# Performance work log

Measured on AMD Instinct MI355X. Metric: run time of the kernel, lower is better.

Reference implementation:

```python
import jax, jax.numpy as jnp
import numpy as np

B, C, F, J = 64, 16, 2048, 25
EMBED, CLASSES, NJ = 64, 5, 12
AFFECT = slice(0, 12)
UNAFFECT = slice(12, 24)


def setup_inputs() -> dict:
    key = jax.random.key(0)
    k0, k1, k2, k3 = jax.random.split(key, 4)
    features = jax.random.normal(k0, (B, C, F, J), dtype=jnp.float32)
    W1 = jax.random.normal(k1, (EMBED, C, NJ), dtype=jnp.float32) * 0.05
    b1 = jnp.zeros((EMBED,), jnp.float32)
    W2 = jax.random.normal(k2, (EMBED, C, NJ), dtype=jnp.float32) * 0.05
    b2 = jnp.zeros((EMBED,), jnp.float32)
    Wl = jax.random.normal(k3, (CLASSES, 16 * EMBED), dtype=jnp.float32) * 0.02
    bl = jnp.zeros((CLASSES,), jnp.float32)
    return {"features": features, "W1": W1, "b1": b1, "W2": W2, "b2": b2, "Wl": Wl, "bl": bl}


def _stat_features(x, proto):
    # x: [b, c, f, j]; single sort shared by min/max/quantiles/median
    f = x.shape[-2]
    xs = jnp.sort(x, axis=-2)

    def quant(p):
        # torch.quantile linear interpolation
        pos = p * (f - 1)
        lo = int(np.floor(pos)); hi = int(np.ceil(pos)); frac = np.float32(pos - lo)
        return xs[..., lo, :] * (1.0 - frac) + xs[..., hi, :] * frac

    s1 = xs[..., 0, :]                       # min
    s2 = xs[..., -1, :]                      # max
    s3 = quant(0.25)
    s4 = xs[..., (f - 1) // 2, :]            # torch.median: lower middle element
    s5 = quant(0.75)
    s6 = jnp.mean(x, axis=-2)
    s7 = jnp.std(x, axis=-2, ddof=1)         # torch.std unbiased
    s8 = s2 - s1
    z = (x - s6[..., None, :]) / s7[..., None, :]
    if proto:
        s9 = jnp.mean(z ** 3, axis=-2)       # skew
    else:
        s9 = jnp.mean(z ** 4, axis=-2) - 3.0  # excess kurtosis
    return jnp.stack([s2, s3, s4, s5, s6, s7, s8, s9], axis=-2)  # [b, c, 8, j]


def _fuse(stat, W, b):
    # Conv2d kernel (1, joints) == contraction over (c, j) per stat row
    out = jnp.einsum('bcsj,ecj->bes', stat, W) + b[None, :, None]
    return out.reshape(out.shape[0], -1)  # flatten (embed, stats) like torch.flatten


def reference(features, W1, b1, W2, b2, Wl, bl):
    affected = features[:, :, :, AFFECT]
    unaffected = features[:, :, :, UNAFFECT]
    stat_af = _stat_features(affected, proto=False)
    stat_ua = _stat_features(unaffected, proto=False)
    # attn=False path (STAT_VA block disabled)
    stat1 = _stat_features(unaffected + affected, proto=True)
    _ = _fuse(stat1, W1, b1)  # stat1 branch only feeds CL loss (get_cl_loss=False)
    stat2 = jnp.concatenate([stat_af, stat_ua], axis=-2)  # [b, c, 16, j]
    flat2 = _fuse(stat2, W2, b2)                          # [b, 16*embed]
    logits = flat2 @ Wl.T + bl
    return logits
```

## Files before the change

### kernel.cpp

```cpp
#include <hip/hip_runtime.h>
#include <hip/hip_bf16.h>
#include <math.h>


#define F_LEN 2048
#define JTOT 25
#define STATS_PER_BC 192
#define LP 2056

__device__ __forceinline__ int swz(int i) {
  return (i & ~31) | ((i + ((i >> 5) << 2)) & 31);
}

template <int PAT>
__device__ __forceinline__ float ds_swz(float v) {
  return __int_as_float(
      __builtin_amdgcn_ds_swizzle(__float_as_int(v), PAT));
}
__device__ __forceinline__ float swzxor(float v, const int lm) {
  switch (lm) {
    case 1:  return ds_swz<0x041F>(v);
    case 2:  return ds_swz<0x081F>(v);
    case 4:  return ds_swz<0x101F>(v);
    case 8:  return ds_swz<0x201F>(v);
    default: return ds_swz<0x401F>(v);
  }
}
__device__ __forceinline__ float wave_sum(float v, int addr32) {
  v += ds_swz<0x041F>(v);
  v += ds_swz<0x081F>(v);
  v += ds_swz<0x101F>(v);
  v += ds_swz<0x201F>(v);
  v += ds_swz<0x401F>(v);
  v += __int_as_float(
      __builtin_amdgcn_ds_bpermute(addr32, __float_as_int(v)));
  return v;
}

__global__ __launch_bounds__(256) void stat_kernel(
    const float* __restrict__ Fp, float* __restrict__ stat2) {
  __shared__ float lds[4 * LP];
  const int g = blockIdx.x;
  const int xcd = g & 7;
  const int mm = g >> 3;
  const int bc = xcd * 128 + mm / 6;
  const int grp = mm % 6;
  const int t = threadIdx.x;
  const int w = t >> 6;
  const int lane = t & 63;
  const int addr32 = ((lane ^ 32) << 2);
  const int j0 = grp * 4;
  float* wlds = lds + w * LP;

  {
    const float* bbase = Fp + (size_t)bc * F_LEN * JTOT + j0;
    const int f0 = t >> 2, jj = t & 3;
    float* ldst = lds + jj * LP;
#pragma unroll
    for (int it = 0; it < 32; ++it) {
      const int f = it * 64 + f0;
      ldst[swz(f)] = bbase[(size_t)f * JTOT + jj];
    }
  }
  __syncthreads();

  float x[32];
  {
    const float4* src4 = (const float4*)wlds;
#pragma unroll
    for (int q = 0; q < 8; ++q) {
      float4 v = src4[lane * 8 + ((lane + q) & 7)];
      x[4 * q] = v.x; x[4 * q + 1] = v.y;
      x[4 * q + 2] = v.z; x[4 * q + 3] = v.w;
    }
  }

  float sum = 0.f;
#pragma unroll
  for (int e = 0; e < 32; ++e) sum += x[e];
  sum = wave_sum(sum, addr32);
  const float m = sum * (1.0f / 2048.0f);

  float c2 = 0.f, c4 = 0.f;
#pragma unroll
  for (int e = 0; e < 32; ++e) {
    float d = x[e] - m;
    float dd = d * d;
    c2 += dd;
    c4 += dd * dd;
  }
  c2 = wave_sum(c2, addr32);
  c4 = wave_sum(c4, addr32);
  const float var = c2 * (1.0f / 2047.0f);
  const float sd = sqrtf(var);
  const float kurt = (c4 * (1.0f / 2048.0f)) / (var * var) - 3.0f;

#pragma unroll
  for (int kp = 1; kp <= 4; ++kp) {
    const int k = 1 << kp;
#pragma unroll
    for (int jp = kp - 1; jp >= 0; --jp) {
      const int st = 1 << jp;
#pragma unroll
      for (int e = 0; e < 32; ++e) {
        if ((e & st) == 0) {
          const bool up = ((e & k) == 0);
          float a = x[e], b = x[e + st];
          float lo2 = fminf(a, b), hi2 = fmaxf(a, b);
          x[e] = up ? lo2 : hi2;
          x[e + st] = up ? hi2 : lo2;
        }
      }
    }
  }

  unsigned Fst = 0u;
#pragma unroll
  for (int kp = 5; kp <= 10; ++kp) {
    const unsigned d = ((lane >> (kp - 5)) & 1) ? 0x80000000u : 0u;
#pragma unroll
    for (int jp = kp - 1; jp >= 5; --jp) {
      const int lm = 1 << (jp - 5);
      const unsigned r = ((lane >> (jp - 5)) & 1) ? 0x80000000u : 0u;
      const unsigned tgt = d ^ r;
      const unsigned fl = tgt ^ Fst;
      Fst = tgt;
#pragma unroll
      for (int e = 0; e < 32; ++e)
        x[e] = __uint_as_float(__float_as_uint(x[e]) ^ fl);
#pragma unroll
      for (int e = 0; e < 32; ++e) {
        float o = swzxor(x[e], lm);
        x[e] = fminf(x[e], -o);
      }
    }
    {
      const unsigned fl = d ^ Fst;
      Fst = d;
#pragma unroll
      for (int e = 0; e < 32; ++e)
        x[e] = __uint_as_float(__float_as_uint(x[e]) ^ fl);
    }
#pragma unroll
    for (int jp = (kp - 1 < 4 ? kp - 1 : 4); jp >= 0; --jp) {
      const int st = 1 << jp;
#pragma unroll
      for (int e = 0; e < 32; ++e) {
        if ((e & st) == 0) {
          float a = x[e], b = x[e + st];
          x[e] = fminf(a, b);
          x[e + st] = fmaxf(a, b);
        }
      }
    }
  }
#pragma unroll
  for (int e = 0; e < 32; ++e)
    x[e] = __uint_as_float(__float_as_uint(x[e]) ^ Fst);

  {
    float4* dst4 = (float4*)wlds;
#pragma unroll
    for (int q = 0; q < 8; ++q) {
      int wq = 8 * lane + ((q + lane) & 7);
      dst4[wq] = make_float4(x[4 * q], x[4 * q + 1], x[4 * q + 2], x[4 * q + 3]);
    }
  }

  const int kk = (lane == 0) ? 511
               : (lane == 1) ? 512
               : (lane == 2) ? 1023
               : (lane == 3) ? 1535 : 1536;
  const int mtot = kk + 1;
  int lo = mtot - 1024; if (lo < 0) lo = 0;
  int hi = (mtot < 1024) ? mtot : 1024;
  for (int it = 0; it < 11; ++it) {
    const bool act = lo < hi;
    const int s = (lo + hi) >> 1;
    const int sa = (s < 1023) ? s : 1023;
    float Av = wlds[swz(sa)];
    Av = (s < 1024) ? Av : INFINITY;
    int bidx = mtot - s - 1;
    bidx = bidx < 0 ? 0 : (bidx > 1023 ? 1023 : bidx);
    const float Bv = wlds[swz(2047 - bidx)];
    const bool gg = act && (Bv > Av);
    if (gg) lo = s + 1;
    else if (act) hi = s;
  }
  float val;
  {
    const int s = lo;
    const int ia = (s - 1 < 0) ? 0 : s - 1;
    const float fa = wlds[swz(ia)];
    const float fromA = (s > 0) ? fa : -INFINITY;
    const int bi = mtot - s - 1;
    const int ib = (bi < 0) ? 0 : bi;
    const float fb = wlds[swz(2047 - ib)];
    const float fromB = (bi >= 0) ? fb : -INFINITY;
    val = fmaxf(fromA, fromB);
  }

  const float a511  = __shfl(val, 0, 64);
  const float a512  = __shfl(val, 1, 64);
  const float amed  = __shfl(val, 2, 64);
  const float a1535 = __shfl(val, 3, 64);
  const float a1536 = __shfl(val, 4, 64);

  if (lane == 0) {
    const float mn = fminf(wlds[swz(0)], wlds[swz(2047)]);
    const float mx = fmaxf(wlds[swz(1023)], wlds[swz(1024)]);
    const float q25 = 0.25f * a511 + 0.75f * a512;
    const float q75 = 0.75f * a1535 + 0.25f * a1536;
    const int j = j0 + w;
    const int jj = (j < 12) ? j : j - 12;
    const int sb = (j < 12) ? 0 : 8;
    float st8[8] = {mx, q25, amed, q75, m, sd, mx - mn, kurt};
    float* o = stat2 + (bc * 16 + sb) * 12 + jj;
#pragma unroll
    for (int s2 = 0; s2 < 8; ++s2) o[s2 * 12] = st8[s2];
  }
}

__global__ __launch_bounds__(256) void fuse_kernel(
    const float* __restrict__ stat2, const float* __restrict__ W2,
    const float* __restrict__ b2, const float* __restrict__ Wl,
    const float* __restrict__ bl, float* __restrict__ out) {
  __shared__ float s_stat[16 * STATS_PER_BC];
  __shared__ float s_flat[1024];
  __shared__ float s_red[4];

  const int b = blockIdx.x;
  const int t = threadIdx.x;

  for (int idx = t; idx < 16 * STATS_PER_BC; idx += 256)
    s_stat[idx] = stat2[b * (16 * STATS_PER_BC) + idx];
  __syncthreads();

  const int e = t & 63;
  const int q = t >> 6;
  float acc[4] = {0.f, 0.f, 0.f, 0.f};
  for (int c = 0; c < 16; ++c) {
    const float* wrow = W2 + (e * 16 + c) * 12;
    const float* srow = s_stat + c * STATS_PER_BC;
#pragma unroll
    for (int jj = 0; jj < 12; ++jj) {
      const float wv = wrow[jj];
#pragma unroll
      for (int ss = 0; ss < 4; ++ss)
        acc[ss] += srow[(q * 4 + ss) * 12 + jj] * wv;
    }
  }
  const float bb = b2[e];
#pragma unroll
  for (int ss = 0; ss < 4; ++ss)
    s_flat[e * 16 + q * 4 + ss] = acc[ss] + bb;
  __syncthreads();

  for (int k = 0; k < 5; ++k) {
    float p = 0.f;
    for (int i = t; i < 1024; i += 256) p += s_flat[i] * Wl[k * 1024 + i];
#pragma unroll
    for (int off = 32; off; off >>= 1) p += __shfl_down(p, off, 64);
    if ((t & 63) == 0) s_red[t >> 6] = p;
    __syncthreads();
    if (t == 0)
      out[b * 5 + k] = s_red[0] + s_red[1] + s_red[2] + s_red[3] + bl[k];
    __syncthreads();
  }
}

extern "C" void kernel_launch(void* const* d_in, const int* in_sizes, int n_in,
                              void* d_out, int out_size, void* d_ws,
                              size_t ws_size, hipStream_t stream) {
  const float* Fp = (const float*)d_in[0];
  const float* W2 = (const float*)d_in[3];
  const float* b2 = (const float*)d_in[4];
  const float* Wl = (const float*)d_in[5];
  const float* bl = (const float*)d_in[6];
  float* out = (float*)d_out;

  float* stat2 = (float*)d_ws;

  stat_kernel<<<6144, 256, 0, stream>>>(Fp, stat2);
  fuse_kernel<<<64, 256, 0, stream>>>(stat2, W2, b2, Wl, bl, out);
}
```

Before: 440.3 us.

## Complete full bitonic sort in registers and drop LDS merge-path quantile search

The bitonic network now runs one more stage across the whole wave, using ds_bpermute for the lane-xor-32 exchange, so all 2048 values end up fully sorted in registers. Order statistics are then read with direct shuffles instead of writing the data back to LDS and doing a merge-path binary search. The load phase now uses vector float4 global reads into a half-sized LDS buffer filled in two passes, and launch bounds request 8 blocks per CU. The aim is to cut LDS footprint and serial search latency and raise occupancy, at the price of an extra full sort stage using a slower cross-half permute.

Result: slower. 462.7 us (+5.1%).

```diff
diff --git a/kernel.cpp b/kernel.cpp
--- a/kernel.cpp
+++ b/kernel.cpp
@@ -8,6 +8,8 @@
 #define STATS_PER_BC 192
 #define LP 2056
 
+typedef float f4a __attribute__((ext_vector_type(4), aligned(4)));
+
 __device__ __forceinline__ int swz(int i) {
   return (i & ~31) | ((i + ((i >> 5) << 2)) & 31);
 }
@@ -17,13 +19,16 @@
   return __int_as_float(
       __builtin_amdgcn_ds_swizzle(__float_as_int(v), PAT));
 }
-__device__ __forceinline__ float swzxor(float v, const int lm) {
+__device__ __forceinline__ float swzxor(float v, const int lm,
+                                        const int addr32) {
   switch (lm) {
     case 1:  return ds_swz<0x041F>(v);
     case 2:  return ds_swz<0x081F>(v);
     case 4:  return ds_swz<0x101F>(v);
     case 8:  return ds_swz<0x201F>(v);
-    default: return ds_swz<0x401F>(v);
+    case 16: return ds_swz<0x401F>(v);
+    default: return __int_as_float(
+        __builtin_amdgcn_ds_bpermute(addr32, __float_as_int(v)));
   }
 }
 __device__ __forceinline__ float wave_sum(float v, int addr32) {
@@ -37,9 +42,22 @@
   return v;
 }
 
-__global__ __launch_bounds__(256) void stat_kernel(
+__device__ __forceinline__ void read_x(const float* wlds, int lane,
+                                       float* x) {
+  const float4* src4 = (const float4*)wlds;
+#pragma unroll
+  for (int q = 0; q < 8; ++q) {
+    float4 v = src4[lane * 8 + ((lane + q) & 7)];
+    x[4 * q] = v.x;
+    x[4 * q + 1] = v.y;
+    x[4 * q + 2] = v.z;
+    x[4 * q + 3] = v.w;
+  }
+}
+
+__global__ __launch_bounds__(256, 8) void stat_kernel(
     const float* __restrict__ Fp, float* __restrict__ stat2) {
-  __shared__ float lds[4 * LP];
+  __shared__ float lds[2 * LP];
   const int g = blockIdx.x;
   const int xcd = g & 7;
   const int mm = g >> 3;
@@ -50,30 +68,37 @@
   const int lane = t & 63;
   const int addr32 = ((lane ^ 32) << 2);
   const int j0 = grp * 4;
-  float* wlds = lds + w * LP;
-
+
+  float vz[8], vw[8];
+  const int rot = (t + ((t >> 5) << 2)) & 31;
+  float* p0 = lds + (t & ~31) + rot;
   {
     const float* bbase = Fp + (size_t)bc * F_LEN * JTOT + j0;
-    const int f0 = t >> 2, jj = t & 3;
-    float* ldst = lds + jj * LP;
-#pragma unroll
-    for (int it = 0; it < 32; ++it) {
-      const int f = it * 64 + f0;
-      ldst[swz(f)] = bbase[(size_t)f * JTOT + jj];
+#pragma unroll
+    for (int it = 0; it < 8; ++it) {
+      const int f = it * 256 + t;
+      f4a v = *reinterpret_cast<const f4a*>(bbase + (size_t)f * JTOT);
+      p0[it * 256] = v.x;
+      p0[LP + it * 256] = v.y;
+      vz[it] = v.z;
+      vw[it] = v.w;
     }
   }
   __syncthreads();
 
   float x[32];
+  if (w < 2) read_x(lds + w * LP, lane, x);
+  __syncthreads();
+
   {
-    const float4* src4 = (const float4*)wlds;
-#pragma unroll
-    for (int q = 0; q < 8; ++q) {
-      float4 v = src4[lane * 8 + ((lane + q) & 7)];
-      x[4 * q] = v.x; x[4 * q + 1] = v.y;
-      x[4 * q + 2] = v.z; x[4 * q + 3] = v.w;
-    }
-  }
+#pragma unroll
+    for (int it = 0; it < 8; ++it) {
+      p0[it * 256] = vz[it];
+      p0[LP + it * 256] = vw[it];
+    }
+  }
+  __syncthreads();
+  if (w >= 2) read_x(lds + (w - 2) * LP, lane, x);
 
   float sum = 0.f;
 #pragma unroll
@@ -116,7 +141,7 @@
 
   unsigned Fst = 0u;
 #pragma unroll
-  for (int kp = 5; kp <= 10; ++kp) {
+  for (int kp = 5; kp <= 11; ++kp) {
     const unsigned d = ((lane >> (kp - 5)) & 1) ? 0x80000000u : 0u;
 #pragma unroll
     for (int jp = kp - 1; jp >= 5; --jp) {
@@ -130,7 +155,7 @@
         x[e] = __uint_as_float(__float_as_uint(x[e]) ^ fl);
 #pragma unroll
       for (int e = 0; e < 32; ++e) {
-        float o = swzxor(x[e], lm);
+        float o = swzxor(x[e], lm, addr32);
         x[e] = fminf(x[e], -o);
       }
     }
@@ -142,7 +167,7 @@
         x[e] = __uint_as_float(__float_as_uint(x[e]) ^ fl);
     }
 #pragma unroll
-    for (int jp = (kp - 1 < 4 ? kp - 1 : 4); jp >= 0; --jp) {
+    for (int jp = 4; jp >= 0; --jp) {
       const int st = 1 << jp;
 #pragma unroll
       for (int e = 0; e < 32; ++e) {
@@ -154,61 +179,16 @@
       }
     }
   }
-#pragma unroll
-  for (int e = 0; e < 32; ++e)
-    x[e] = __uint_as_float(__float_as_uint(x[e]) ^ Fst);
-
-  {
-    float4* dst4 = (float4*)wlds;
-#pragma unroll
-    for (int q = 0; q < 8; ++q) {
-      int wq = 8 * lane + ((q + lane) & 7);
-      dst4[wq] = make_float4(x[4 * q], x[4 * q + 1], x[4 * q + 2], x[4 * q + 3]);
-    }
-  }
-
-  const int kk = (lane == 0) ? 511
-               : (lane == 1) ? 512
-               : (lane == 2) ? 1023
-               : (lane == 3) ? 1535 : 1536;
-  const int mtot = kk + 1;
-  int lo = mtot - 1024; if (lo < 0) lo = 0;
-  int hi = (mtot < 1024) ? mtot : 1024;
-  for (int it = 0; it < 11; ++it) {
-    const bool act = lo < hi;
-    const int s = (lo + hi) >> 1;
-    const int sa = (s < 1023) ? s : 1023;
-    float Av = wlds[swz(sa)];
-    Av = (s < 1024) ? Av : INFINITY;
-    int bidx = mtot - s - 1;
-    bidx = bidx < 0 ? 0 : (bidx > 1023 ? 1023 : bidx);
-    const float Bv = wlds[swz(2047 - bidx)];
-    const bool gg = act && (Bv > Av);
-    if (gg) lo = s + 1;
-    else if (act) hi = s;
-  }
-  float val;
-  {
-    const int s = lo;
-    const int ia = (s - 1 < 0) ? 0 : s - 1;
-    const float fa = wlds[swz(ia)];
-    const float fromA = (s > 0) ? fa : -INFINITY;
-    const int bi = mtot - s - 1;
-    const int ib = (bi < 0) ? 0 : bi;
-    const float fb = wlds[swz(2047 - ib)];
-    const float fromB = (bi >= 0) ? fb : -INFINITY;
-    val = fmaxf(fromA, fromB);
-  }
-
-  const float a511  = __shfl(val, 0, 64);
-  const float a512  = __shfl(val, 1, 64);
-  const float amed  = __shfl(val, 2, 64);
-  const float a1535 = __shfl(val, 3, 64);
-  const float a1536 = __shfl(val, 4, 64);
+
+  const float mn = __shfl(x[0], 0, 64);
+  const float a511 = __shfl(x[31], 15, 64);
+  const float a512 = __shfl(x[0], 16, 64);
+  const float amed = __shfl(x[31], 31, 64);
+  const float a1535 = __shfl(x[31], 47, 64);
+  const float a1536 = __shfl(x[0], 48, 64);
+  const float mx = __shfl(x[31], 63, 64);
 
   if (lane == 0) {
-    const float mn = fminf(wlds[swz(0)], wlds[swz(2047)]);
-    const float mx = fmaxf(wlds[swz(1023)], wlds[swz(1024)]);
     const float q25 = 0.25f * a511 + 0.75f * a512;
     const float q75 = 0.75f * a1535 + 0.25f * a1536;
     const int j = j0 + w;
```
